# Kernel tuning notes

Hardware: AMD Instinct MI355X
Metric: run time of the kernel (lower is better)

Reference implementation:

```python
import math
import jax, jax.numpy as jnp
import numpy as np

N = 100000      # nodes
E = 3200000     # edges (avg degree 32)
NFEAT = 512
NH = 256
NC = 40
NL = 8
ALPHA = 0.1
LAMDA = 0.5


def setup_inputs() -> dict:
    key = jax.random.key(0)
    ks = jax.random.split(key, 9)
    features = jax.random.normal(ks[0], (N, NFEAT), jnp.float32)
    edge_rows = jax.random.randint(ks[1], (E,), 0, N, jnp.int32)
    edge_cols = jax.random.randint(ks[2], (E,), 0, N, jnp.int32)
    # scale by 1/avg_degree so aggregated features stay O(1) (mimics normalized adjacency)
    edge_vals = jax.random.uniform(ks[3], (E,), jnp.float32) / 32.0
    # fcs[0]: nn.Linear(nfeat, nhidden) default init U(-1/sqrt(in), 1/sqrt(in))
    b1 = 1.0 / math.sqrt(NFEAT)
    W_in = jax.random.uniform(ks[4], (NFEAT, NH), jnp.float32, -b1, b1)
    b_in = jax.random.uniform(ks[5], (NH,), jnp.float32, -b1, b1)
    # GraphConvolution weights: U(-1/sqrt(out), 1/sqrt(out))
    bw = 1.0 / math.sqrt(NH)
    conv_weights = jax.random.uniform(ks[6], (NL, NH, NH), jnp.float32, -bw, bw)
    # fcs[1]: nn.Linear(nhidden, nclass)
    b2 = 1.0 / math.sqrt(NH)
    W_out = jax.random.uniform(ks[7], (NH, NC), jnp.float32, -b2, b2)
    b_out = jax.random.uniform(ks[8], (NC,), jnp.float32, -b2, b2)
    return {
        "features": features,
        "edge_rows": edge_rows,
        "edge_cols": edge_cols,
        "edge_vals": edge_vals,
        "W_in": W_in,
        "b_in": b_in,
        "conv_weights": conv_weights,
        "W_out": W_out,
        "b_out": b_out,
    }


def reference(features, edge_rows, edge_cols, edge_vals, W_in, b_in, conv_weights, W_out, b_out):
    # dropout p=0 in eval -> identity
    h = jax.nn.relu(features @ W_in + b_in)  # [N, NH]
    h0 = h
    for i in range(NL):
        theta = math.log(LAMDA / (i + 1) + 1.0)
        # SpMM: hi = G @ h via gather + segment-sum over destination rows
        hi = jax.ops.segment_sum(edge_vals[:, None] * h[edge_cols], edge_rows, num_segments=N)
        support = (1.0 - ALPHA) * hi + ALPHA * h0  # variant=False -> r == support
        h = jax.nn.relu(theta * (support @ conv_weights[i]) + (1.0 - theta) * support)
    return h @ W_out + b_out  # [N, NC]
```

## Files before the change

kernel.cpp:

```cpp
#include <hip/hip_runtime.h>
#include <hip/hip_fp16.h>
#include <math.h>

#define NNODE   100000
#define NEDGE   3200000
#define NFEAT   512
#define NH      256
#define NC      40
#define NL      8

#define SCAN_B  256

typedef _Float16 f16x8 __attribute__((ext_vector_type(8)));
typedef float    f32x4 __attribute__((ext_vector_type(4)));

__global__ void count_deg_kernel(const int* __restrict__ rows, int* __restrict__ deg, int e) {
    int i = blockIdx.x * blockDim.x + threadIdx.x;
    if (i < e) atomicAdd(&deg[rows[i]], 1);
}

__global__ void scan_pass1(const int* __restrict__ deg, int* __restrict__ rowptr,
                           int* __restrict__ bsums, int n) {
    __shared__ int sm[SCAN_B];
    int i = blockIdx.x * SCAN_B + threadIdx.x;
    int v = (i < n) ? deg[i] : 0;
    sm[threadIdx.x] = v;
    __syncthreads();
    for (int off = 1; off < SCAN_B; off <<= 1) {
        int t = (threadIdx.x >= (unsigned)off) ? sm[threadIdx.x - off] : 0;
        __syncthreads();
        sm[threadIdx.x] += t;
        __syncthreads();
    }
    if (i < n) rowptr[i] = sm[threadIdx.x] - v;
    if (threadIdx.x == SCAN_B - 1) bsums[blockIdx.x] = sm[threadIdx.x];
}

__global__ void scan_pass2(int* __restrict__ bsums, int nb) {
    __shared__ int sm[512];
    int tid = threadIdx.x;
    int v = (tid < nb) ? bsums[tid] : 0;
    sm[tid] = v;
    __syncthreads();
    for (int off = 1; off < 512; off <<= 1) {
        int t = (tid >= off) ? sm[tid - off] : 0;
        __syncthreads();
        sm[tid] += t;
        __syncthreads();
    }
    if (tid < nb) bsums[tid] = sm[tid] - v;
}

__global__ void scan_pass3(int* __restrict__ rowptr, const int* __restrict__ bsums,
                           int* __restrict__ cursor, int n, int total) {
    int i = blockIdx.x * blockDim.x + threadIdx.x;
    if (i < n) {
        int v = rowptr[i] + bsums[i / SCAN_B];
        rowptr[i] = v;
        cursor[i] = v;
    }
    if (i == 0) rowptr[n] = total;
}

__global__ void scatter_edges_kernel(const int* __restrict__ rows, const int* __restrict__ cols,
                                     const float* __restrict__ vals, int* __restrict__ cursor,
                                     int2* __restrict__ csr_cv, int e) {
    int i = blockIdx.x * blockDim.x + threadIdx.x;
    if (i < e) {
        int r = rows[i];
        int p = atomicAdd(&cursor[r], 1);
        csr_cv[p] = make_int2(cols[i], __float_as_int(vals[i]));
    }
}

__device__ inline float4 dec8(uint2 p) {
    __half2 h01 = *(__half2*)&p.x;
    __half2 h23 = *(__half2*)&p.y;
    float2 f01 = __half22float2(h01);
    float2 f23 = __half22float2(h23);
    return make_float4(f01.x, f01.y, f23.x, f23.y);
}

__device__ inline void gload16(const void* g, void* l) {
    __builtin_amdgcn_global_load_lds((const __attribute__((address_space(1))) void*)g,
                                     (__attribute__((address_space(3))) void*)l,
                                     16, 0, 0);
}

__global__ void convert_win(const float* __restrict__ in, __half* __restrict__ out) {
    int idx = blockIdx.x * blockDim.x + threadIdx.x;
    if (idx < NFEAT * NH) {
        int k = idx >> 8;
        int n = idx & 255;
        out[n * NFEAT + k] = __float2half(in[idx]);
    }
}

__global__ void convert_convw(const float* __restrict__ in, __half* __restrict__ out) {
    int idx = blockIdx.x * blockDim.x + threadIdx.x;
    if (idx < NL * NH * NH) {
        int l = idx >> 16;
        int rem = idx & 65535;
        int k = rem >> 8;
        int n = rem & 255;
        out[(size_t)l * 65536 + n * 256 + k] = __float2half(in[idx]);
    }
}

__global__ __launch_bounds__(256) void spmm_kernel(
    const int* __restrict__ rowptr, const int2* __restrict__ csr_cv,
    const __half* __restrict__ h16, const __half* __restrict__ h016,
    __half* __restrict__ sup16, int n)
{
    int lane = threadIdx.x & 63;
    int r = blockIdx.x * 4 + (threadIdx.x >> 6);
    if (r >= n) return;
    int e0 = rowptr[r], e1 = rowptr[r + 1];
    const uint2* hv = (const uint2*)h16;
    float4 acc = make_float4(0.f, 0.f, 0.f, 0.f);
    int e = e0;
    for (; e + 4 <= e1; e += 4) {
        int2 a0 = csr_cv[e],     a1 = csr_cv[e + 1];
        int2 a2 = csr_cv[e + 2], a3 = csr_cv[e + 3];
        float v0 = __int_as_float(a0.y), v1 = __int_as_float(a1.y);
        float v2 = __int_as_float(a2.y), v3 = __int_as_float(a3.y);
        uint2 p0 = hv[(size_t)a0.x * 64 + lane];
        uint2 p1 = hv[(size_t)a1.x * 64 + lane];
        uint2 p2 = hv[(size_t)a2.x * 64 + lane];
        uint2 p3 = hv[(size_t)a3.x * 64 + lane];
        float4 x0 = dec8(p0), x1 = dec8(p1), x2 = dec8(p2), x3 = dec8(p3);
        acc.x += v0 * x0.x + v1 * x1.x + v2 * x2.x + v3 * x3.x;
        acc.y += v0 * x0.y + v1 * x1.y + v2 * x2.y + v3 * x3.y;
        acc.z += v0 * x0.z + v1 * x1.z + v2 * x2.z + v3 * x3.z;
        acc.w += v0 * x0.w + v1 * x1.w + v2 * x2.w + v3 * x3.w;
    }
    for (; e < e1; ++e) {
        int2 a = csr_cv[e];
        float v = __int_as_float(a.y);
        float4 x = dec8(hv[(size_t)a.x * 64 + lane]);
        acc.x += v * x.x; acc.y += v * x.y; acc.z += v * x.z; acc.w += v * x.w;
    }
    float4 s0 = dec8(((const uint2*)h016)[(size_t)r * 64 + lane]);
    float4 o;
    o.x = 0.9f * acc.x + 0.1f * s0.x;
    o.y = 0.9f * acc.y + 0.1f * s0.y;
    o.z = 0.9f * acc.z + 0.1f * s0.z;
    o.w = 0.9f * acc.w + 0.1f * s0.w;
    __half2 ha = __floats2half2_rn(o.x, o.y);
    __half2 hb = __floats2half2_rn(o.z, o.w);
    uint2 pk;
    pk.x = *(unsigned*)&ha;
    pk.y = *(unsigned*)&hb;
    ((uint2*)sup16)[(size_t)r * 64 + lane] = pk;
}

template <bool AFLOAT>
__global__ __launch_bounds__(256) void mfma_gemm(
    const void* __restrict__ Aptr, const __half* __restrict__ BT,
    const float* __restrict__ bias, const __half* __restrict__ Csrc16,
    __half* __restrict__ out16, int M, int K,
    float theta, float omt, int mode)
{
    __shared__ __align__(16) char smem[32768];
    const int tid  = threadIdx.x;
    const int lane = tid & 63;
    const int w    = tid >> 6;
    const int wr   = w >> 1, wc = w & 1;
    const int bm0  = blockIdx.x * 128;
    const int bn0  = blockIdx.y * 128;
    const size_t strideB = (size_t)K * 2;

    f32x4 acc[4][4];
    #pragma unroll
    for (int m = 0; m < 4; ++m)
        #pragma unroll
        for (int n = 0; n < 4; ++n)
            acc[m][n] = (f32x4)0.f;

    auto stage = [&](int kt, int buf) {
        if constexpr (AFLOAT) {
            const float* A32 = (const float*)Aptr;
            #pragma unroll
            for (int it = 0; it < 4; ++it) {
                int idx = tid + it * 256;
                int r   = idx >> 3;
                int t   = idx & 7;
                int grow = bm0 + r; if (grow >= M) grow = M - 1;
                float4 f = *(const float4*)&A32[(size_t)grow * K + kt * 32 + t * 4];
                __half2 a = __floats2half2_rn(f.x, f.y);
                __half2 b = __floats2half2_rn(f.z, f.w);
                uint2 pk;
                pk.x = *(unsigned*)&a;
                pk.y = *(unsigned*)&b;
                int slot = t >> 1;
                int off  = r * 64 + ((slot ^ ((r >> 1) & 3)) << 4) + (t & 1) * 8;
                *(uint2*)(smem + buf * 16384 + off) = pk;
            }
        } else {
            const char* A16 = (const char*)Aptr;
            const long k0b = (long)kt * 64;
            #pragma unroll
            for (int i = 0; i < 2; ++i) {
                int ia  = w * 2 + i;
                int row = ia * 16 + (lane >> 2);
                int q   = (lane & 3) * 16;
                int qs  = q ^ (((row >> 1) & 3) << 4);
                int grow = bm0 + row; if (grow >= M) grow = M - 1;
                const char* g = A16 + (size_t)grow * strideB + k0b + qs;
                gload16(g, smem + buf * 16384 + ia * 1024);
            }
        }
        {
            const long k0b = (long)kt * 64;
            #pragma unroll
            for (int i = 0; i < 2; ++i) {
                int ia  = w * 2 + i;
                int row = ia * 16 + (lane >> 2);
                int q   = (lane & 3) * 16;
                int qs  = q ^ (((row >> 1) & 3) << 4);
                int gcol = bn0 + row;
                const char* g = (const char*)BT + (size_t)gcol * strideB + k0b + qs;
                gload16(g, smem + buf * 16384 + 8192 + ia * 1024);
            }
        }
    };

    auto compute = [&](int buf) {
        const char* As = smem + buf * 16384;
        const char* Bs = As + 8192;
        const int q = (lane >> 4) * 16;
        f16x8 af[4], bf[4];
        #pragma unroll
        for (int m = 0; m < 4; ++m) {
            int row = wr * 64 + m * 16 + (lane & 15);
            af[m] = *(const f16x8*)(As + row * 64 + (q ^ (((row >> 1) & 3) << 4)));
        }
        #pragma unroll
        for (int n = 0; n < 4; ++n) {
            int col = wc * 64 + n * 16 + (lane & 15);
            bf[n] = *(const f16x8*)(Bs + col * 64 + (q ^ (((col >> 1) & 3) << 4)));
        }
        #pragma unroll
        for (int m = 0; m < 4; ++m)
            #pragma unroll
            for (int n = 0; n < 4; ++n)
                acc[m][n] = __builtin_amdgcn_mfma_f32_16x16x32_f16(af[m], bf[n], acc[m][n], 0, 0, 0);
    };

    const int nkt = K >> 5;
    stage(0, 0);
    __syncthreads();
    for (int kt = 0; kt < nkt; ++kt) {
        if (kt + 1 < nkt) stage(kt + 1, (kt + 1) & 1);
        compute(kt & 1);
        __syncthreads();
    }

    #pragma unroll
    for (int m = 0; m < 4; ++m) {
        int rbase = bm0 + wr * 64 + m * 16 + (lane >> 4) * 4;
        #pragma unroll
        for (int r = 0; r < 4; ++r) {
            int grow = rbase + r;
            if (grow >= M) continue;
            #pragma unroll
            for (int n = 0; n < 4; ++n) {
                int gcol = bn0 + wc * 64 + n * 16 + (lane & 15);
                float x = acc[m][n][r];
                if (mode == 0) {
                    x = fmaxf(x + bias[gcol], 0.f);
                } else {
                    float s = __half2float(Csrc16[(size_t)grow * 256 + gcol]);
                    x = fmaxf(theta * x + omt * s, 0.f);
                }
                out16[(size_t)grow * 256 + gcol] = __float2half(x);
            }
        }
    }
}

#define BM 128
#define BN 64
#define BK 16

__global__ __launch_bounds__(256) void gemm_out_kernel(
    const __half* __restrict__ A16, const float* __restrict__ B,
    const float* __restrict__ bias, float* __restrict__ out32,
    int M, int Nn, int K)
{
    __shared__ float As[BK][BM + 4];
    __shared__ float Bs[BK][BN + 4];
    int tid = threadIdx.x;
    int tx = tid & 15;
    int ty = tid >> 4;
    int bm0 = blockIdx.x * BM;
    int bn0 = blockIdx.y * BN;

    float acc[8][4];
    #pragma unroll
    for (int i = 0; i < 8; ++i)
        #pragma unroll
        for (int j = 0; j < 4; ++j) acc[i][j] = 0.f;

    for (int k0 = 0; k0 < K; k0 += BK) {
        #pragma unroll
        for (int r = 0; r < 2; ++r) {
            int idx = tid + r * 256;
            int m   = idx >> 2;
            int kk  = (idx & 3) * 4;
            int gm  = bm0 + m;
            float4 f = make_float4(0.f, 0.f, 0.f, 0.f);
            if (gm < M) f = dec8(*(const uint2*)&A16[(size_t)gm * K + k0 + kk]);
            As[kk + 0][m] = f.x;
            As[kk + 1][m] = f.y;
            As[kk + 2][m] = f.z;
            As[kk + 3][m] = f.w;
        }
        {
            int kk = tid >> 4;
            int n4 = (tid & 15) * 4;
            int gn = bn0 + n4;
            const float* brow = &B[(size_t)(k0 + kk) * Nn];
            Bs[kk][n4 + 0] = (gn + 0 < Nn) ? brow[gn + 0] : 0.f;
            Bs[kk][n4 + 1] = (gn + 1 < Nn) ? brow[gn + 1] : 0.f;
            Bs[kk][n4 + 2] = (gn + 2 < Nn) ? brow[gn + 2] : 0.f;
            Bs[kk][n4 + 3] = (gn + 3 < Nn) ? brow[gn + 3] : 0.f;
        }
        __syncthreads();
        #pragma unroll
        for (int kk = 0; kk < BK; ++kk) {
            float a[8], b[4];
            #pragma unroll
            for (int i = 0; i < 8; ++i) a[i] = As[kk][ty * 8 + i];
            #pragma unroll
            for (int j = 0; j < 4; ++j) b[j] = Bs[kk][tx * 4 + j];
            #pragma unroll
            for (int i = 0; i < 8; ++i)
                #pragma unroll
                for (int j = 0; j < 4; ++j)
                    acc[i][j] += a[i] * b[j];
        }
        __syncthreads();
    }

    #pragma unroll
    for (int i = 0; i < 8; ++i) {
        int m = bm0 + ty * 8 + i;
        if (m >= M) continue;
        int n0 = bn0 + tx * 4;
        #pragma unroll
        for (int j = 0; j < 4; ++j) {
            int n = n0 + j;
            if (n < Nn) out32[(size_t)m * Nn + n] = acc[i][j] + bias[n];
        }
    }
}

extern "C" void kernel_launch(void* const* d_in, const int* in_sizes, int n_in,
                              void* d_out, int out_size, void* d_ws, size_t ws_size,
                              hipStream_t stream) {
    const float* features = (const float*)d_in[0];
    const int*   erows    = (const int*)d_in[1];
    const int*   ecols    = (const int*)d_in[2];
    const float* evals    = (const float*)d_in[3];
    const float* W_in     = (const float*)d_in[4];
    const float* b_in     = (const float*)d_in[5];
    const float* convW    = (const float*)d_in[6];
    const float* W_out    = (const float*)d_in[7];
    const float* b_out    = (const float*)d_in[8];
    float* out = (float*)d_out;

    const int n = NNODE;
    const int e = NEDGE;

    char* w = (char*)d_ws;
    auto alloc = [&](size_t bytes) -> void* {
        void* p = (void*)w;
        w += (bytes + 255) & ~(size_t)255;
        return p;
    };
    __half* h0_16   = (__half*)alloc((size_t)n * NH * 2);
    __half* hb_16   = (__half*)alloc((size_t)n * NH * 2);
    __half* sup16   = (__half*)alloc((size_t)n * NH * 2);
    __half* WtIn16  = (__half*)alloc((size_t)NFEAT * NH * 2);
    __half* convWt16= (__half*)alloc((size_t)NL * NH * NH * 2);
    int*    rowptr  = (int*)alloc((size_t)(n + 1) * 4);
    int*    cursor  = (int*)alloc((size_t)n * 4);
    int*    bsums   = (int*)alloc(4096 * 4);
    int2*   csr_cv  = (int2*)alloc((size_t)e * 8);

    convert_win<<<(NFEAT * NH + 255) / 256, 256, 0, stream>>>(W_in, WtIn16);
    convert_convw<<<(NL * NH * NH + 255) / 256, 256, 0, stream>>>(convW, convWt16);

    hipMemsetAsync(cursor, 0, (size_t)n * 4, stream);
    count_deg_kernel<<<(e + 255) / 256, 256, 0, stream>>>(erows, cursor, e);
    int nb = (n + SCAN_B - 1) / SCAN_B;
    scan_pass1<<<nb, SCAN_B, 0, stream>>>(cursor, rowptr, bsums, n);
    scan_pass2<<<1, 512, 0, stream>>>(bsums, nb);
    scan_pass3<<<nb, SCAN_B, 0, stream>>>(rowptr, bsums, cursor, n, e);
    scatter_edges_kernel<<<(e + 255) / 256, 256, 0, stream>>>(
        erows, ecols, evals, cursor, csr_cv, e);

    dim3 gmm((n + 127) / 128, 2);
    mfma_gemm<true><<<gmm, 256, 0, stream>>>(features, WtIn16, b_in, nullptr,
                                             h0_16, n, NFEAT, 0.f, 0.f, 0);

    const __half* hcur16 = h0_16;
    for (int i = 0; i < NL; ++i) {
        spmm_kernel<<<(n + 3) / 4, 256, 0, stream>>>(rowptr, csr_cv,
                                                     hcur16, h0_16, sup16, n);
        double th = log(0.5 / (double)(i + 1) + 1.0);
        mfma_gemm<false><<<gmm, 256, 0, stream>>>(sup16, convWt16 + (size_t)i * NH * NH,
                                                  nullptr, sup16, hb_16,
                                                  n, NH, (float)th, (float)(1.0 - th), 1);
        hcur16 = hb_16;
    }

    dim3 gout((n + BM - 1) / BM, (NC + BN - 1) / BN);
    gemm_out_kernel<<<gout, 256, 0, stream>>>(hb_16, W_out, b_out, out, n, NC, NH);
}
```

Before: 3.175 ms.

## Split edge scatter into row-range passes and deepen SpMM gather unrolling

The CSR build now runs as eight passes over the edge list, each scattering only the edges whose destination row falls in one slice of rows. This keeps the random atomic and write traffic on a smaller window of cursor and CSR memory at a time, with better cache locality. The cost is re-reading the row array eight times. The SpMM inner loop now issues eight gathers per iteration with all loads hoisted ahead of the math, plus a 2-wide remainder loop, to keep more memory requests in flight. This raises register pressure.

```diff
diff --git a/kernel.cpp b/kernel.cpp
--- a/kernel.cpp
+++ b/kernel.cpp
@@ -10,6 +10,7 @@
 #define NL      8
 
 #define SCAN_B  256
+#define NPASS   8
 
 typedef _Float16 f16x8 __attribute__((ext_vector_type(8)));
 typedef float    f32x4 __attribute__((ext_vector_type(4)));
@@ -62,15 +63,15 @@
     if (i == 0) rowptr[n] = total;
 }
 
-__global__ void scatter_edges_kernel(const int* __restrict__ rows, const int* __restrict__ cols,
-                                     const float* __restrict__ vals, int* __restrict__ cursor,
-                                     int2* __restrict__ csr_cv, int e) {
+__global__ void scatter_pass_kernel(const int* __restrict__ rows, const int* __restrict__ cols,
+                                    const float* __restrict__ vals, int* __restrict__ cursor,
+                                    int2* __restrict__ csr_cv, int e, int lo, int hi) {
     int i = blockIdx.x * blockDim.x + threadIdx.x;
-    if (i < e) {
-        int r = rows[i];
-        int p = atomicAdd(&cursor[r], 1);
-        csr_cv[p] = make_int2(cols[i], __float_as_int(vals[i]));
-    }
+    if (i >= e) return;
+    int r = rows[i];
+    if (r < lo || r >= hi) return;
+    int p = atomicAdd(&cursor[r], 1);
+    csr_cv[p] = make_int2(cols[i], __float_as_int(vals[i]));
 }
 
 __device__ inline float4 dec8(uint2 p) {
@@ -119,22 +120,35 @@
     const uint2* hv = (const uint2*)h16;
     float4 acc = make_float4(0.f, 0.f, 0.f, 0.f);
     int e = e0;
-    for (; e + 4 <= e1; e += 4) {
-        int2 a0 = csr_cv[e],     a1 = csr_cv[e + 1];
-        int2 a2 = csr_cv[e + 2], a3 = csr_cv[e + 3];
-        float v0 = __int_as_float(a0.y), v1 = __int_as_float(a1.y);
-        float v2 = __int_as_float(a2.y), v3 = __int_as_float(a3.y);
+    #pragma unroll 1
+    for (; e + 8 <= e1; e += 8) {
+        int2 a[8];
+        uint2 p[8];
+        #pragma unroll
+        for (int j = 0; j < 8; ++j) a[j] = csr_cv[e + j];
+        #pragma unroll
+        for (int j = 0; j < 8; ++j) p[j] = hv[(size_t)a[j].x * 64 + lane];
+        #pragma unroll
+        for (int j = 0; j < 8; ++j) {
+            float v = __int_as_float(a[j].y);
+            float4 x = dec8(p[j]);
+            acc.x += v * x.x; acc.y += v * x.y;
+            acc.z += v * x.z; acc.w += v * x.w;
+        }
+    }
+    #pragma unroll 1
+    for (; e + 2 <= e1; e += 2) {
+        int2 a0 = csr_cv[e], a1 = csr_cv[e + 1];
         uint2 p0 = hv[(size_t)a0.x * 64 + lane];
         uint2 p1 = hv[(size_t)a1.x * 64 + lane];
-        uint2 p2 = hv[(size_t)a2.x * 64 + lane];
-        uint2 p3 = hv[(size_t)a3.x * 64 + lane];
-        float4 x0 = dec8(p0), x1 = dec8(p1), x2 = dec8(p2), x3 = dec8(p3);
-        acc.x += v0 * x0.x + v1 * x1.x + v2 * x2.x + v3 * x3.x;
-        acc.y += v0 * x0.y + v1 * x1.y + v2 * x2.y + v3 * x3.y;
-        acc.z += v0 * x0.z + v1 * x1.z + v2 * x2.z + v3 * x3.z;
-        acc.w += v0 * x0.w + v1 * x1.w + v2 * x2.w + v3 * x3.w;
-    }
-    for (; e < e1; ++e) {
+        float v0 = __int_as_float(a0.y), v1 = __int_as_float(a1.y);
+        float4 x0 = dec8(p0), x1 = dec8(p1);
+        acc.x += v0 * x0.x + v1 * x1.x;
+        acc.y += v0 * x0.y + v1 * x1.y;
+        acc.z += v0 * x0.z + v1 * x1.z;
+        acc.w += v0 * x0.w + v1 * x1.w;
+    }
+    if (e < e1) {
         int2 a = csr_cv[e];
         float v = __int_as_float(a.y);
         float4 x = dec8(hv[(size_t)a.x * 64 + lane]);
@@ -398,8 +412,15 @@
     scan_pass1<<<nb, SCAN_B, 0, stream>>>(cursor, rowptr, bsums, n);
     scan_pass2<<<1, 512, 0, stream>>>(bsums, nb);
     scan_pass3<<<nb, SCAN_B, 0, stream>>>(rowptr, bsums, cursor, n, e);
-    scatter_edges_kernel<<<(e + 255) / 256, 256, 0, stream>>>(
-        erows, ecols, evals, cursor, csr_cv, e);
+    {
+        int chunk = (n + NPASS - 1) / NPASS;
+        for (int p = 0; p < NPASS; ++p) {
+            int lo = p * chunk;
+            int hi = min(n, lo + chunk);
+            scatter_pass_kernel<<<(e + 255) / 256, 256, 0, stream>>>(
+                erows, ecols, evals, cursor, csr_cv, e, lo, hi);
+        }
+    }
 
     dim3 gmm((n + 127) / 128, 2);
     mfma_gemm<true><<<gmm, 256, 0, stream>>>(features, WtIn16, b_in, nullptr,
```

Result: no change. 3.126 ms (-1.6%).
